# Performance work log

Measured on AMD Instinct MI355X. Metric: run time of the kernel, lower is better.

Reference implementation:

```python
import jax, jax.numpy as jnp
import numpy as np
import math

D_MODEL = 1024
N_HEADS = 16
DH = D_MODEL // N_HEADS
THETA = 10000.0


def _rope_tables(S):
    # freqs: (dh/2,)
    inv_freq = 1.0 / (THETA ** (jnp.arange(0, DH, 2, dtype=jnp.float32) / DH))
    ang = jnp.arange(S, dtype=jnp.float32)[:, None] * inv_freq[None, :]  # (S, dh/2)
    cos = jnp.concatenate([jnp.cos(ang), jnp.cos(ang)], axis=-1)  # (S, dh)
    sin = jnp.concatenate([jnp.sin(ang), jnp.sin(ang)], axis=-1)
    return cos, sin


def _apply_rope(x, cos, sin):
    # x: (B, S, H, dh); rotate-half RoPE
    x1, x2 = jnp.split(x, 2, axis=-1)
    rot = jnp.concatenate([-x2, x1], axis=-1)
    c = cos[None, :, None, :]
    s = sin[None, :, None, :]
    return x * c + rot * s


def setup_inputs() -> dict:
    key = jax.random.key(0)
    k1, k2, k3 = jax.random.split(key, 3)
    x = jax.random.normal(k1, (4, 2048, D_MODEL), dtype=jnp.float32)
    qkv = 0.01 * jax.random.normal(k2, (3 * D_MODEL, D_MODEL), dtype=jnp.float32)
    wo = 0.01 * jax.random.normal(k3, (D_MODEL, D_MODEL), dtype=jnp.float32)
    return {"x": x, "qkv": qkv, "wo": wo}


def reference(x, qkv, wo):
    B, S, D = x.shape
    QKV = x @ qkv.T  # (B, S, 3D)
    Q, K, V = jnp.split(QKV, 3, axis=-1)
    q = Q.reshape(B, S, N_HEADS, DH)
    k = K.reshape(B, S, N_HEADS, DH)
    v = V.reshape(B, S, N_HEADS, DH)
    cos, sin = _rope_tables(S)
    q = _apply_rope(q, cos, sin)
    k = _apply_rope(k, cos, sin)
    # (B, H, S, dh)
    q = q.transpose(0, 2, 1, 3)
    k = k.transpose(0, 2, 1, 3)
    v = v.transpose(0, 2, 1, 3)
    scores = jnp.einsum("bhsd,bhtd->bhst", q, k) / math.sqrt(float(DH))
    mask = jnp.tril(jnp.ones((S, S), dtype=scores.dtype))
    scores = scores * mask
    # faithful to original: any exact-zero entry (masked or incidental) -> -inf
    scores = jnp.where(scores == 0.0, -jnp.inf, scores)
    attn = jax.nn.softmax(scores, axis=-1)
    out = jnp.einsum("bhst,bhtd->bhsd", attn, v)  # (B, H, S, dh)
    out = out.transpose(0, 2, 1, 3).reshape(B, S, D)
    return out @ wo.T
```

## Files before the change

### kernel.cpp

```cpp
#include <hip/hip_runtime.h>
#include <math.h>

typedef __bf16 bf16x8 __attribute__((ext_vector_type(8)));
typedef __bf16 bf16x4 __attribute__((ext_vector_type(4)));
typedef float  floatx4 __attribute__((ext_vector_type(4)));
typedef float  floatx2 __attribute__((ext_vector_type(2)));

#define AS1(p) ((__attribute__((address_space(1))) void*)(p))
#define AS3(p) ((__attribute__((address_space(3))) void*)(p))

#define MASKV (-1.0e30f)
#define SOFTMAX_SCALE_LOG2 0.1803368801111244f
#define ROPE_LOG2F 0.4152410118609203f

#define BARRIER do { __builtin_amdgcn_sched_barrier(0); \
                     __builtin_amdgcn_s_barrier(); \
                     __builtin_amdgcn_sched_barrier(0); } while (0)

__global__ __launch_bounds__(256)
void cvt3_kernel(const float* __restrict__ x, const float* __restrict__ qkv,
                 const float* __restrict__ wo, __bf16* __restrict__ xb,
                 __bf16* __restrict__ qkvb, __bf16* __restrict__ wob,
                 float* __restrict__ rt)
{
    const int bi = blockIdx.x;
    if (bi >= 12288) {
        const int e0 = (bi - 12288) * 1024 + threadIdx.x * 4;
#pragma unroll
        for (int j = 0; j < 4; ++j) {
            const int e = e0 + j;
            const int s = e >> 5, d = e & 31;
            const float f = exp2f(-(float)d * ROPE_LOG2F);
            float sn, cs;
            sincosf((float)s * f, &sn, &cs);
            floatx2 t; t[0] = cs; t[1] = sn;
            *(floatx2*)(rt + e * 2) = t;
        }
        return;
    }
    const float* src;
    __bf16* dst;
    int base;
    if (bi < 8192)       { src = x;   dst = xb;   base = bi * 1024; }
    else if (bi < 11264) { src = qkv; dst = qkvb; base = (bi - 8192) * 1024; }
    else                 { src = wo;  dst = wob;  base = (bi - 11264) * 1024; }

    const int i = base + threadIdx.x * 4;
    const floatx4 v = *(const floatx4*)(src + i);
    bf16x4 o;
    o[0] = (__bf16)v[0]; o[1] = (__bf16)v[1];
    o[2] = (__bf16)v[2]; o[3] = (__bf16)v[3];
    *(bf16x4*)(dst + i) = o;
}

__device__ __forceinline__ void gemm_pipe(const __bf16* __restrict__ Ap,
                                          const __bf16* __restrict__ Bp,
                                          const int m0, const int n0,
                                          __bf16* smem, floatx4 (&acc)[4][4])
{
    const int tid  = threadIdx.x;
    const int wave = tid >> 6;
    const int lane = tid & 63;
    const int quad = lane >> 4;
    const int l16  = lane & 15;
    const int wr   = wave >> 2;
    const int wc   = wave & 3;

    const int arow = wr * 32 + l16;
    const int brow = (wc & 1) * 64 + l16;
    const int bsel = (wc >> 1) * 8192;
    const int swz  = (l16 & 7) << 4;
    int coff[2];
    coff[0] = (( (quad << 4))        ^ swz) >> 1;
    coff[1] = ((64 | (quad << 4))    ^ swz) >> 1;

    auto stageA = [&](int buf, int h, int k0) {
        const int o = tid << 4;
        const int r = o >> 7;
        const int c = (o & 127) ^ ((r & 7) << 4);
        const __bf16* src = Ap + (size_t)(m0 + h * 64 + r) * 1024 + k0 + (c >> 1);
        __builtin_amdgcn_global_load_lds(AS1(src),
            AS3(smem + buf * 24576 + h * 4096 + wave * 512), 16, 0, 0);
    };
    auto stageB = [&](int buf, int h, int k0) {
#pragma unroll
        for (int q = 0; q < 2; ++q) {
            const int o = (q * 512 + tid) << 4;
            const int r = o >> 7;
            const int c = (o & 127) ^ ((r & 7) << 4);
            const __bf16* src = Bp + (size_t)(n0 + h * 128 + r) * 1024 + k0 + (c >> 1);
            __builtin_amdgcn_global_load_lds(AS1(src),
                AS3(smem + buf * 24576 + 8192 + h * 8192 + (q * 8 + wave) * 512), 16, 0, 0);
        }
    };

#define RDA(P, qm, fm, ks) (*(const bf16x8*)(smem + (P) * 24576 + (qm) * 4096 \
                             + ((arow + (fm) * 16) << 6) + coff[ks]))
#define RDB(P, g, ks)      (*(const bf16x8*)(smem + (P) * 24576 + 8192 + bsel \
                             + ((brow + (g) * 16) << 6) + coff[ks]))
#define MFMA16(MB, AH) do { \
    _Pragma("unroll") for (int fm_ = 0; fm_ < 2; ++fm_) \
    _Pragma("unroll") for (int g_ = 0; g_ < 4; ++g_) \
    _Pragma("unroll") for (int ks_ = 0; ks_ < 2; ++ks_) \
        acc[(MB) + fm_][g_] = __builtin_amdgcn_mfma_f32_16x16x32_bf16( \
            AH[fm_][ks_], b[g_][ks_], acc[(MB) + fm_][g_], 0, 0, 0); \
} while (0)

    stageA(0, 0, 0);  stageA(0, 1, 0);  stageB(0, 0, 0);  stageB(0, 1, 0);
    stageA(1, 0, 64); stageA(1, 1, 64); stageB(1, 0, 64); stageB(1, 1, 64);
    asm volatile("s_waitcnt vmcnt(6)" ::: "memory");
    BARRIER;

    bf16x8 a0[2][2], a1[2][2], b[4][2];

#define TILE3(JT) do { \
    const int P_ = (JT) % 3, T_ = ((JT) + 2) % 3; \
    const int kn_ = ((JT) + 2) * 64; \
    _Pragma("unroll") for (int fm_ = 0; fm_ < 2; ++fm_) \
    _Pragma("unroll") for (int ks_ = 0; ks_ < 2; ++ks_) a0[fm_][ks_] = RDA(P_, 0, fm_, ks_); \
    _Pragma("unroll") for (int g_ = 0; g_ < 4; ++g_) \
    _Pragma("unroll") for (int ks_ = 0; ks_ < 2; ++ks_) b[g_][ks_] = RDB(P_, g_, ks_); \
    _Pragma("unroll") for (int fm_ = 0; fm_ < 2; ++fm_) \
    _Pragma("unroll") for (int ks_ = 0; ks_ < 2; ++ks_) a1[fm_][ks_] = RDA(P_, 1, fm_, ks_); \
    if ((JT) + 2 < 16) { stageA(T_, 0, kn_); stageA(T_, 1, kn_); \
                         stageB(T_, 0, kn_); stageB(T_, 1, kn_); } \
    __builtin_amdgcn_s_setprio(1); \
    MFMA16(0, a0); MFMA16(2, a1); \
    __builtin_amdgcn_s_setprio(0); \
    if ((JT) + 2 < 16)      { asm volatile("s_waitcnt vmcnt(6)" ::: "memory"); } \
    else if ((JT) + 1 < 16) { asm volatile("s_waitcnt vmcnt(0)" ::: "memory"); } \
    BARRIER; \
} while (0)

    TILE3(0);  TILE3(1);  TILE3(2);  TILE3(3);
    TILE3(4);  TILE3(5);  TILE3(6);  TILE3(7);
    TILE3(8);  TILE3(9);  TILE3(10); TILE3(11);
    TILE3(12); TILE3(13); TILE3(14); TILE3(15);

#undef TILE3
#undef RDA
#undef RDB
#undef MFMA16
}

__global__ __launch_bounds__(512, 2)
void gemm_rope_kernel(const __bf16* __restrict__ A, const __bf16* __restrict__ BT,
                      __bf16* __restrict__ Qr, __bf16* __restrict__ Kr,
                      __bf16* __restrict__ Vt, const float* __restrict__ rt)
{
    extern __shared__ __align__(16) __bf16 smem[];
    const int id  = blockIdx.x;
    const int xcd = id & 7, lid = id >> 3;
    const int tm  = xcd * 8 + lid / 12;
    const int tn  = lid % 12;
    const int m0  = tm * 128, n0 = tn * 256;

    floatx4 acc[4][4] = {};
    gemm_pipe(A, BT, m0, n0, smem, acc);

    const int tid  = threadIdx.x;
    const int wave = tid >> 6;
    const int lane = tid & 63;
    const int quad = lane >> 4, l16 = lane & 15;
    const int wr   = wave >> 2, wc = wave & 3;

    const int gn0    = n0 + wc * 64;
    const int region = gn0 >> 10;
    const int h      = (gn0 >> 6) & 15;

    if (region == 2) {
#pragma unroll
        for (int f = 0; f < 4; ++f) {
            const int gm = m0 + (f >> 1) * 64 + wr * 32 + (f & 1) * 16 + quad * 4;
            const int b = gm >> 11, s = gm & 2047;
#pragma unroll
            for (int g = 0; g < 4; ++g) {
                const int d = g * 16 + l16;
                bf16x4 w;
#pragma unroll
                for (int r = 0; r < 4; ++r) w[r] = (__bf16)acc[f][g][r];
                *(bf16x4*)(Vt + ((size_t)(b * 16 + h) * 64 + d) * 2048 + s) = w;
            }
        }
    } else {
        __bf16* dst = region ? Kr : Qr;
        const float sc = region ? 1.0f : SOFTMAX_SCALE_LOG2;
#pragma unroll
        for (int g = 0; g < 2; ++g) {
            const int d1 = g * 16 + l16;
#pragma unroll
            for (int f = 0; f < 4; ++f) {
                const int gm0 = m0 + (f >> 1) * 64 + wr * 32 + (f & 1) * 16 + quad * 4;
                const int b = gm0 >> 11, s0 = gm0 & 2047;
#pragma unroll
                for (int r = 0; r < 4; ++r) {
                    const floatx2 t = *(const floatx2*)(rt + ((s0 + r) * 32 + d1) * 2);
                    const float a1 = acc[f][g][r];
                    const float a2 = acc[f][g + 2][r];
                    __bf16* row = dst + ((size_t)((b * 16 + h) * 2048 + s0 + r)) * 64;
                    row[d1]      = (__bf16)((a1 * t[0] - a2 * t[1]) * sc);
                    row[d1 + 32] = (__bf16)((a2 * t[0] + a1 * t[1]) * sc);
                }
            }
        }
    }
}

__global__ __launch_bounds__(512, 2)
void gemm_bt_kernel(const __bf16* __restrict__ A, const __bf16* __restrict__ BT,
                    float* __restrict__ C)
{
    extern __shared__ __align__(16) __bf16 smem[];
    const int id  = blockIdx.x;
    const int xcd = id & 7, lid = id >> 3;
    const int tm  = xcd * 8 + (lid >> 2);
    const int tn  = lid & 3;
    const int m0  = tm * 128, n0 = tn * 256;

    floatx4 acc[4][4] = {};
    gemm_pipe(A, BT, m0, n0, smem, acc);

    const int tid  = threadIdx.x;
    const int wave = tid >> 6, lane = tid & 63;
    const int quad = lane >> 4, l16 = lane & 15;
    const int wr   = wave >> 2, wc = wave & 3;

#pragma unroll
    for (int f = 0; f < 4; ++f) {
        const int row = m0 + (f >> 1) * 64 + wr * 32 + (f & 1) * 16 + quad * 4;
#pragma unroll
        for (int g = 0; g < 4; ++g) {
            const int col = n0 + wc * 64 + g * 16 + l16;
#pragma unroll
            for (int r = 0; r < 4; ++r)
                C[(size_t)(row + r) * 1024 + col] = acc[f][g][r];
        }
    }
}

__global__ __launch_bounds__(256, 4)
void attn_kernel(const __bf16* __restrict__ Qr, const __bf16* __restrict__ Kr,
                 const __bf16* __restrict__ Vt, __bf16* __restrict__ ctx)
{
    __shared__ __align__(16) __bf16 Ks[64 * 64];
    __shared__ __align__(16) __bf16 Vs[64 * 64];
    __shared__ __align__(16) __bf16 plds[4][16 * 72];

    const int bh   = blockIdx.x;
    const int b    = bh >> 4, h = bh & 15;
    const int tid  = threadIdx.x;
    const int wave = tid >> 6;
    const int lane = tid & 63;
    const int quad = lane >> 4, l16 = lane & 15;
    const int sw   = l16 & 7;

    const __bf16* Qb = Qr + (size_t)bh * 2048 * 64;
    const __bf16* Kb = Kr + (size_t)bh * 2048 * 64;
    const __bf16* Vb = Vt + (size_t)bh * 64 * 2048;
    __bf16* Pw = &plds[wave][0];

    const int row0 = tid >> 3, jg0 = (tid & 7) ^ (row0 & 7);
    const int c1   = 256 + tid;
    const int row1 = c1 >> 3, jg1 = (c1 & 7) ^ (row1 & 7);

    const __bf16* pK0 = Kb + (size_t)row0 * 64 + jg0 * 8;
    const __bf16* pK1 = Kb + (size_t)row1 * 64 + jg1 * 8;
    const __bf16* pV0 = Vb + (size_t)row0 * 2048 + jg0 * 8;
    const __bf16* pV1 = Vb + (size_t)row1 * 2048 + jg1 * 8;

    const int tiles[2] = { (int)blockIdx.y, 31 - (int)blockIdx.y };

    for (int pass = 0; pass < 2; ++pass) {
        const int tq    = tiles[pass];
        const int q0    = tq * 64 + wave * 16;
        const int qa    = q0 + l16;
        const int ntile = tq + 1;

        bf16x8 bq[2];
#pragma unroll
        for (int t = 0; t < 2; ++t)
            bq[t] = *(const bf16x8*)(Qb + (q0 + l16) * 64 + t * 32 + quad * 8);

        floatx4 o[4] = {};
        float lpart = 0.f;

        bf16x8 rk0 = *(const bf16x8*)pK0;
        bf16x8 rk1 = *(const bf16x8*)pK1;
        bf16x8 rv0 = *(const bf16x8*)pV0;
        bf16x8 rv1 = *(const bf16x8*)pV1;

        __syncthreads();

        for (int t = 0; t < ntile; ++t) {
            asm volatile("s_waitcnt vmcnt(0)" ::: "memory");
            *(bf16x8*)(Ks + tid * 8)        = rk0;
            *(bf16x8*)(Ks + 2048 + tid * 8) = rk1;
            *(bf16x8*)(Vs + tid * 8)        = rv0;
            *(bf16x8*)(Vs + 2048 + tid * 8) = rv1;
            asm volatile("s_waitcnt lgkmcnt(0)" ::: "memory");
            BARRIER;

            if (t + 1 < ntile) {
                rk0 = *(const bf16x8*)(pK0 + (size_t)(t + 1) * 4096);
                rk1 = *(const bf16x8*)(pK1 + (size_t)(t + 1) * 4096);
                rv0 = *(const bf16x8*)(pV0 + (t + 1) * 64);
                rv1 = *(const bf16x8*)(pV1 + (t + 1) * 64);
            }

            const int  kt     = t * 64;
            const bool masked = (t == ntile - 1);

            floatx4 s[4] = {};
            __builtin_amdgcn_s_setprio(1);
#pragma unroll
            for (int st = 0; st < 4; ++st) {
                bf16x8 ka0 = *(const bf16x8*)(Ks + (st * 16 + l16) * 64 + ((0 + quad) ^ sw) * 8);
                bf16x8 ka1 = *(const bf16x8*)(Ks + (st * 16 + l16) * 64 + ((4 + quad) ^ sw) * 8);
                s[st] = __builtin_amdgcn_mfma_f32_16x16x32_bf16(ka0, bq[0], s[st], 0, 0, 0);
                s[st] = __builtin_amdgcn_mfma_f32_16x16x32_bf16(ka1, bq[1], s[st], 0, 0, 0);
            }
            __builtin_amdgcn_s_setprio(0);

#pragma unroll
            for (int st = 0; st < 4; ++st) {
                bf16x4 w;
#pragma unroll
                for (int r = 0; r < 4; ++r) {
                    float v = s[st][r];
                    if (masked) {
                        const int key = kt + st * 16 + quad * 4 + r;
                        v = (key > qa) ? MASKV : v;
                    }
                    const float p = __builtin_amdgcn_exp2f(v);
                    lpart += p;
                    w[r] = (__bf16)p;
                }
                *(bf16x4*)(Pw + l16 * 72 + st * 16 + quad * 4) = w;
            }

            asm volatile("s_waitcnt lgkmcnt(0)" ::: "memory");
            bf16x8 ap0 = *(const bf16x8*)(Pw + l16 * 72 + quad * 8);
            bf16x8 ap1 = *(const bf16x8*)(Pw + l16 * 72 + 32 + quad * 8);

            __builtin_amdgcn_s_setprio(1);
#pragma unroll
            for (int nt = 0; nt < 4; ++nt) {
                bf16x8 bv0 = *(const bf16x8*)(Vs + (nt * 16 + l16) * 64 + ((0 + quad) ^ sw) * 8);
                bf16x8 bv1 = *(const bf16x8*)(Vs + (nt * 16 + l16) * 64 + ((4 + quad) ^ sw) * 8);
                o[nt] = __builtin_amdgcn_mfma_f32_16x16x32_bf16(ap0, bv0, o[nt], 0, 0, 0);
                o[nt] = __builtin_amdgcn_mfma_f32_16x16x32_bf16(ap1, bv1, o[nt], 0, 0, 0);
            }
            __builtin_amdgcn_s_setprio(0);

            BARRIER;
        }

        float l = lpart;
        l += __shfl_xor(l, 16, 64);
        l += __shfl_xor(l, 32, 64);
        float lr[4];
#pragma unroll
        for (int r = 0; r < 4; ++r)
            lr[r] = __shfl(l, quad * 4 + r, 64);
#pragma unroll
        for (int nt = 0; nt < 4; ++nt)
#pragma unroll
            for (int r = 0; r < 4; ++r) {
                const int srow = q0 + quad * 4 + r;
                const float inv_l = 1.0f / fmaxf(lr[r], 1e-20f);
                ctx[((size_t)(b * 2048 + srow)) * 1024 + h * 64 + nt * 16 + l16] =
                    (__bf16)(o[nt][r] * inv_l);
            }
    }
}

extern "C" void kernel_launch(void* const* d_in, const int* in_sizes, int n_in,
                              void* d_out, int out_size, void* d_ws, size_t ws_size,
                              hipStream_t stream)
{
    const float* x   = (const float*)d_in[0];
    const float* qkv = (const float*)d_in[1];
    const float* wo  = (const float*)d_in[2];
    float* out = (float*)d_out;

    char* ws = (char*)d_ws;
    const size_t MB = 1024 * 1024;
    __bf16* xb   = (__bf16*)(ws);
    __bf16* qkvb = (__bf16*)(ws + 16 * MB);
    __bf16* wob  = (__bf16*)(ws + 22 * MB);
    __bf16* Qr   = (__bf16*)(ws + 24 * MB);
    __bf16* Kr   = (__bf16*)(ws + 40 * MB);
    __bf16* Vt   = (__bf16*)(ws + 56 * MB);
    __bf16* ctx  = (__bf16*)(ws + 72 * MB);
    float*  rt   = (float*) (ws + 88 * MB);

    hipFuncSetAttribute((const void*)gemm_rope_kernel,
                        hipFuncAttributeMaxDynamicSharedMemorySize, 147456);
    hipFuncSetAttribute((const void*)gemm_bt_kernel,
                        hipFuncAttributeMaxDynamicSharedMemorySize, 147456);

    cvt3_kernel<<<12352, 256, 0, stream>>>(x, qkv, wo, xb, qkvb, wob, rt);
    gemm_rope_kernel<<<768, 512, 147456, stream>>>(xb, qkvb, Qr, Kr, Vt, rt);
    attn_kernel<<<dim3(64, 16), 256, 0, stream>>>(Qr, Kr, Vt, ctx);
    gemm_bt_kernel<<<256, 512, 147456, stream>>>(ctx, wob, out);
}
```

Baseline: 224.9 us.

## Use 256x256 tiles with split-half pipelined staging in QKV GEMM

Rewrites the QKV projection GEMM to compute 256x256 output tiles per block instead of 128x256, halving the grid from 768 to 384 blocks. It adds its own double-buffered pipeline that stages A and B in halves interleaved with quarter-tile MFMA groups, using 128 KB of LDS. The aim is more reuse per loaded byte and better overlap of loads with MFMA work. In exchange, each thread holds twice as many accumulators, which risks register pressure or spills, and the smaller grid may leave compute units idle or unevenly loaded.

```diff
diff --git a/kernel.cpp b/kernel.cpp
--- a/kernel.cpp
+++ b/kernel.cpp
@@ -51,6 +51,168 @@
     o[0] = (__bf16)v[0]; o[1] = (__bf16)v[1];
     o[2] = (__bf16)v[2]; o[3] = (__bf16)v[3];
     *(bf16x4*)(dst + i) = o;
+}
+
+__global__ __launch_bounds__(512, 2)
+void gemm_rope_kernel(const __bf16* __restrict__ A, const __bf16* __restrict__ BT,
+                      __bf16* __restrict__ Qr, __bf16* __restrict__ Kr,
+                      __bf16* __restrict__ Vt, const float* __restrict__ rt)
+{
+    extern __shared__ __align__(16) __bf16 smem[];
+    const int id  = blockIdx.x;
+    const int xcd = id & 7, lid = id >> 3;
+    const int tm  = xcd * 4 + lid / 12;
+    const int tn  = lid % 12;
+    const int m0  = tm * 256, n0 = tn * 256;
+
+    const int tid  = threadIdx.x;
+    const int wave = tid >> 6;
+    const int lane = tid & 63;
+    const int quad = lane >> 4;
+    const int l16  = lane & 15;
+    const int wr   = wave >> 2;
+    const int wc   = wave & 3;
+
+    const int swz = (l16 & 7) << 4;
+    int coff[2];
+    coff[0] = (( (quad << 4))     ^ swz) >> 1;
+    coff[1] = ((64 | (quad << 4)) ^ swz) >> 1;
+
+    const int aoff = wr * 1024 + l16 * 64;
+    const int boff = wc * 2048 + l16 * 64;
+
+    auto stageAH = [&](int bufQ, int h, int k0) {
+#pragma unroll
+        for (int q = 0; q < 2; ++q) {
+            const int o  = (q * 512 + tid) << 4;
+            const int lr = o >> 7;
+            const int c  = (o & 127) ^ ((lr & 7) << 4);
+            const __bf16* src = A + (size_t)(m0 + h * 128 + lr) * 1024 + k0 + (c >> 1);
+            __builtin_amdgcn_global_load_lds(AS1(src),
+                AS3(smem + bufQ * 32768 + h * 8192 + (q * 8 + wave) * 512), 16, 0, 0);
+        }
+    };
+    auto stageBH = [&](int bufQ, int h, int k0) {
+#pragma unroll
+        for (int q = 0; q < 2; ++q) {
+            const int o  = (q * 512 + tid) << 4;
+            const int lr = o >> 7;
+            const int c  = (o & 127) ^ ((lr & 7) << 4);
+            const int gr = n0 + ((lr >> 4) * 2 + h) * 16 + (lr & 15);
+            const __bf16* src = BT + (size_t)gr * 1024 + k0 + (c >> 1);
+            __builtin_amdgcn_global_load_lds(AS1(src),
+                AS3(smem + bufQ * 32768 + 16384 + h * 8192 + (q * 8 + wave) * 512), 16, 0, 0);
+        }
+    };
+
+    floatx4 acc[8][4] = {};
+    bf16x8 a[4][2], b[4][2];
+
+#define RDA(P, f, ks) (*(const bf16x8*)(smem + (P) * 32768 + ((f) >> 2) * 8192 \
+                        + ((f) & 3) * 2048 + aoff + coff[ks]))
+#define RDB(P, g, ks) (*(const bf16x8*)(smem + (P) * 32768 + 16384 + ((g) & 1) * 8192 \
+                        + ((g) >> 1) * 1024 + boff + coff[ks]))
+#define MFQ(FB, G0, G1) do { \
+    _Pragma("unroll") for (int fm_ = 0; fm_ < 4; ++fm_) \
+    _Pragma("unroll") for (int ks_ = 0; ks_ < 2; ++ks_) { \
+        acc[(FB)+fm_][G0] = __builtin_amdgcn_mfma_f32_16x16x32_bf16( \
+            a[fm_][ks_], b[G0][ks_], acc[(FB)+fm_][G0], 0, 0, 0); \
+        acc[(FB)+fm_][G1] = __builtin_amdgcn_mfma_f32_16x16x32_bf16( \
+            a[fm_][ks_], b[G1][ks_], acc[(FB)+fm_][G1], 0, 0, 0); \
+    } \
+} while (0)
+
+    stageAH(0, 0, 0); stageBH(0, 0, 0); stageBH(0, 1, 0); stageAH(0, 1, 0);
+    asm volatile("s_waitcnt vmcnt(4)" ::: "memory");
+    BARRIER;
+
+#define GTILE(JT) do { \
+    const int P_ = (JT) & 1, Q_ = 1 - P_; \
+    const int kn_ = ((JT) + 1) * 64; \
+     \
+    _Pragma("unroll") for (int fm_ = 0; fm_ < 4; ++fm_) \
+    _Pragma("unroll") for (int ks_ = 0; ks_ < 2; ++ks_) a[fm_][ks_] = RDA(P_, fm_, ks_); \
+    _Pragma("unroll") for (int ks_ = 0; ks_ < 2; ++ks_) { \
+        b[0][ks_] = RDB(P_, 0, ks_); b[2][ks_] = RDB(P_, 2, ks_); } \
+    if ((JT) + 1 < 16) { stageAH(Q_, 0, kn_); \
+                         asm volatile("s_waitcnt vmcnt(4)" ::: "memory"); } \
+    else               { asm volatile("s_waitcnt vmcnt(2)" ::: "memory"); } \
+    BARRIER; \
+    asm volatile("s_waitcnt lgkmcnt(0)" ::: "memory"); \
+    __builtin_amdgcn_s_setprio(1); MFQ(0, 0, 2); __builtin_amdgcn_s_setprio(0); \
+     \
+    _Pragma("unroll") for (int ks_ = 0; ks_ < 2; ++ks_) { \
+        b[1][ks_] = RDB(P_, 1, ks_); b[3][ks_] = RDB(P_, 3, ks_); } \
+    if ((JT) + 1 < 16) { stageBH(Q_, 0, kn_); \
+                         asm volatile("s_waitcnt vmcnt(4)" ::: "memory"); } \
+    else               { asm volatile("s_waitcnt vmcnt(0)" ::: "memory"); } \
+    BARRIER; \
+    asm volatile("s_waitcnt lgkmcnt(0)" ::: "memory"); \
+    __builtin_amdgcn_s_setprio(1); MFQ(0, 1, 3); __builtin_amdgcn_s_setprio(0); \
+     \
+    _Pragma("unroll") for (int fm_ = 0; fm_ < 4; ++fm_) \
+    _Pragma("unroll") for (int ks_ = 0; ks_ < 2; ++ks_) a[fm_][ks_] = RDA(P_, 4 + fm_, ks_); \
+    if ((JT) + 1 < 16) stageBH(Q_, 1, kn_); \
+    BARRIER; \
+    asm volatile("s_waitcnt lgkmcnt(0)" ::: "memory"); \
+    __builtin_amdgcn_s_setprio(1); MFQ(4, 1, 3); __builtin_amdgcn_s_setprio(0); \
+     \
+    if ((JT) + 1 < 16) { stageAH(Q_, 1, kn_); \
+                         asm volatile("s_waitcnt vmcnt(4)" ::: "memory"); } \
+    BARRIER; \
+    __builtin_amdgcn_s_setprio(1); MFQ(4, 0, 2); __builtin_amdgcn_s_setprio(0); \
+} while (0)
+
+    GTILE(0);  GTILE(1);  GTILE(2);  GTILE(3);
+    GTILE(4);  GTILE(5);  GTILE(6);  GTILE(7);
+    GTILE(8);  GTILE(9);  GTILE(10); GTILE(11);
+    GTILE(12); GTILE(13); GTILE(14); GTILE(15);
+
+#undef GTILE
+#undef MFQ
+#undef RDA
+#undef RDB
+
+    const int gn0    = n0 + wc * 64;
+    const int region = gn0 >> 10;
+    const int h      = (gn0 >> 6) & 15;
+
+    if (region == 2) {
+#pragma unroll
+        for (int f = 0; f < 8; ++f) {
+            const int gm = m0 + (f >> 2) * 128 + ((f & 3) * 2 + wr) * 16 + quad * 4;
+            const int bb = gm >> 11, s = gm & 2047;
+#pragma unroll
+            for (int g = 0; g < 4; ++g) {
+                const int d = g * 16 + l16;
+                bf16x4 w;
+#pragma unroll
+                for (int r = 0; r < 4; ++r) w[r] = (__bf16)acc[f][g][r];
+                *(bf16x4*)(Vt + ((size_t)(bb * 16 + h) * 64 + d) * 2048 + s) = w;
+            }
+        }
+    } else {
+        __bf16* dst = region ? Kr : Qr;
+        const float sc = region ? 1.0f : SOFTMAX_SCALE_LOG2;
+#pragma unroll
+        for (int g = 0; g < 2; ++g) {
+            const int d1 = g * 16 + l16;
+#pragma unroll
+            for (int f = 0; f < 8; ++f) {
+                const int gm0 = m0 + (f >> 2) * 128 + ((f & 3) * 2 + wr) * 16 + quad * 4;
+                const int bb = gm0 >> 11, s0 = gm0 & 2047;
+#pragma unroll
+                for (int r = 0; r < 4; ++r) {
+                    const floatx2 t = *(const floatx2*)(rt + ((s0 + r) * 32 + d1) * 2);
+                    const float a1 = acc[f][g][r];
+                    const float a2 = acc[f][g + 2][r];
+                    __bf16* row = dst + ((size_t)((bb * 16 + h) * 2048 + s0 + r)) * 64;
+                    row[d1]      = (__bf16)((a1 * t[0] - a2 * t[1]) * sc);
+                    row[d1 + 32] = (__bf16)((a2 * t[0] + a1 * t[1]) * sc);
+                }
+            }
+        }
+    }
 }
 
 __device__ __forceinline__ void gemm_pipe(const __bf16* __restrict__ Ap,
@@ -144,69 +306,6 @@
 }
 
 __global__ __launch_bounds__(512, 2)
-void gemm_rope_kernel(const __bf16* __restrict__ A, const __bf16* __restrict__ BT,
-                      __bf16* __restrict__ Qr, __bf16* __restrict__ Kr,
-                      __bf16* __restrict__ Vt, const float* __restrict__ rt)
-{
-    extern __shared__ __align__(16) __bf16 smem[];
-    const int id  = blockIdx.x;
-    const int xcd = id & 7, lid = id >> 3;
-    const int tm  = xcd * 8 + lid / 12;
-    const int tn  = lid % 12;
-    const int m0  = tm * 128, n0 = tn * 256;
-
-    floatx4 acc[4][4] = {};
-    gemm_pipe(A, BT, m0, n0, smem, acc);
-
-    const int tid  = threadIdx.x;
-    const int wave = tid >> 6;
-    const int lane = tid & 63;
-    const int quad = lane >> 4, l16 = lane & 15;
-    const int wr   = wave >> 2, wc = wave & 3;
-
-    const int gn0    = n0 + wc * 64;
-    const int region = gn0 >> 10;
-    const int h      = (gn0 >> 6) & 15;
-
-    if (region == 2) {
-#pragma unroll
-        for (int f = 0; f < 4; ++f) {
-            const int gm = m0 + (f >> 1) * 64 + wr * 32 + (f & 1) * 16 + quad * 4;
-            const int b = gm >> 11, s = gm & 2047;
-#pragma unroll
-            for (int g = 0; g < 4; ++g) {
-                const int d = g * 16 + l16;
-                bf16x4 w;
-#pragma unroll
-                for (int r = 0; r < 4; ++r) w[r] = (__bf16)acc[f][g][r];
-                *(bf16x4*)(Vt + ((size_t)(b * 16 + h) * 64 + d) * 2048 + s) = w;
-            }
-        }
-    } else {
-        __bf16* dst = region ? Kr : Qr;
-        const float sc = region ? 1.0f : SOFTMAX_SCALE_LOG2;
-#pragma unroll
-        for (int g = 0; g < 2; ++g) {
-            const int d1 = g * 16 + l16;
-#pragma unroll
-            for (int f = 0; f < 4; ++f) {
-                const int gm0 = m0 + (f >> 1) * 64 + wr * 32 + (f & 1) * 16 + quad * 4;
-                const int b = gm0 >> 11, s0 = gm0 & 2047;
-#pragma unroll
-                for (int r = 0; r < 4; ++r) {
-                    const floatx2 t = *(const floatx2*)(rt + ((s0 + r) * 32 + d1) * 2);
-                    const float a1 = acc[f][g][r];
-                    const float a2 = acc[f][g + 2][r];
-                    __bf16* row = dst + ((size_t)((b * 16 + h) * 2048 + s0 + r)) * 64;
-                    row[d1]      = (__bf16)((a1 * t[0] - a2 * t[1]) * sc);
-                    row[d1 + 32] = (__bf16)((a2 * t[0] + a1 * t[1]) * sc);
-                }
-            }
-        }
-    }
-}
-
-__global__ __launch_bounds__(512, 2)
 void gemm_bt_kernel(const __bf16* __restrict__ A, const __bf16* __restrict__ BT,
                     float* __restrict__ C)
 {
@@ -395,12 +494,12 @@
     float*  rt   = (float*) (ws + 88 * MB);
 
     hipFuncSetAttribute((const void*)gemm_rope_kernel,
-                        hipFuncAttributeMaxDynamicSharedMemorySize, 147456);
+                        hipFuncAttributeMaxDynamicSharedMemorySize, 131072);
     hipFuncSetAttribute((const void*)gemm_bt_kernel,
                         hipFuncAttributeMaxDynamicSharedMemorySize, 147456);
 
     cvt3_kernel<<<12352, 256, 0, stream>>>(x, qkv, wo, xb, qkvb, wob, rt);
-    gemm_rope_kernel<<<768, 512, 147456, stream>>>(xb, qkvb, Qr, Kr, Vt, rt);
+    gemm_rope_kernel<<<384, 512, 131072, stream>>>(xb, qkvb, Qr, Kr, Vt, rt);
     attn_kernel<<<dim3(64, 16), 256, 0, stream>>>(Qr, Kr, Vt, ctx);
     gemm_bt_kernel<<<256, 512, 147456, stream>>>(ctx, wob, out);
 }
```

After: 221.9 us. No clear change (-1.4%).
